# Kernel tuning notes

Hardware: AMD Instinct MI355X
Metric: run time of the kernel (lower is better)

The kernel has to match this reference:

```python
import jax, jax.numpy as jnp
import numpy as np

N = 2048
D0, D1, D2 = 33, 33, 65
O = 128

def setup_inputs() -> dict:
    key = jax.random.key(0)
    k0, k1, k2, kw = jax.random.split(key, 4)
    x0 = jax.random.normal(k0, (N, D0), dtype=jnp.float32)
    x1 = jax.random.normal(k1, (N, D1), dtype=jnp.float32)
    x2 = jax.random.normal(k2, (N, D2), dtype=jnp.float32)
    # xavier_normal for weight_tensor of shape input_sizes + (output_size,):
    # fan_in = D0*D1*D2 treated as receptive field? torch xavier on 4D tensor uses
    # fan_in = shape[1]*receptive, but for faithfulness of *math* any gaussian init works;
    # use std = sqrt(2/(fan_in+fan_out)) with fan computed as torch does for >2D:
    # fan_in = shape[1]*shape[2]*shape[3]? torch: fan_in = size(1)*prod(size()[2:]),
    # fan_out = size(0)*prod(size()[2:]).
    recept = D2 * O
    fan_in = D1 * recept
    fan_out = D0 * recept
    std = float(np.sqrt(2.0 / (fan_in + fan_out)))
    weight_tensor = jax.random.normal(kw, (D0, D1, D2, O), dtype=jnp.float32) * std
    bias = jnp.zeros((O,), dtype=jnp.float32)
    return {"x0": x0, "x1": x1, "x2": x2, "weight_tensor": weight_tensor, "bias": bias}

def reference(x0, x1, x2, weight_tensor, bias):
    # fusion_tensor[n,a,b,c] = x0[n,a]*x1[n,b]*x2[n,c]  (chained outer products)
    # output[n,o] = sum_{a,b,c} fusion[n,a,b,c] * W[a,b,c,o] + bias; dropout(p=0) is identity.
    # Expressed as one fused einsum (same math, avoids HBM round-trip of the big intermediate).
    out = jnp.einsum('na,nb,nc,abco->no', x0, x1, x2, weight_tensor)
    out = jax.nn.relu(out + bias)
    return out
```

## Files before the change

### kernel.cpp

```cpp
#include <hip/hip_runtime.h>
#include <hip/hip_bf16.h>

typedef __attribute__((ext_vector_type(8))) short bf16x8;
typedef __attribute__((ext_vector_type(4))) float f32x4;

#define U_LD 2176
#define K_REAL 2145
#define NKT 34
#define DIM0 33
#define DIM1 33
#define DIM2 65
#define NROW 2048
#define OO 128

__device__ __forceinline__ unsigned short f2bf(float f) {
  union { float f; unsigned u; } v; v.f = f;
  unsigned r = v.u + 0x7fffu + ((v.u >> 16) & 1u);
  return (unsigned short)(r >> 16);
}

#define GLOAD_LDS16(SRC, DST) \
  __builtin_amdgcn_global_load_lds((const __attribute__((address_space(1))) void*)(SRC), \
                                   (__attribute__((address_space(3))) void*)(DST), 16, 0, 0)

__global__ __launch_bounds__(256) void prep_u_kernel(const float* __restrict__ x1,
                                                     const float* __restrict__ x2,
                                                     ushort* __restrict__ U) {
  __shared__ float s1[DIM1], s2[DIM2];
  int n = blockIdx.x;
  int tid = threadIdx.x;
  if (tid < DIM1) s1[tid] = x1[n * DIM1 + tid];
  int t2 = tid - DIM1;
  if (t2 >= 0 && t2 < DIM2) s2[t2] = x2[n * DIM2 + t2];
  __syncthreads();
  for (int k8 = tid; k8 < U_LD / 8; k8 += 256) {
    union { ushort us[8]; uint4 v; } pk;
#pragma unroll
    for (int j = 0; j < 8; ++j) {
      int k = k8 * 8 + j;
      float val = 0.f;
      if (k < K_REAL) { int b = k / DIM2; int c = k - b * DIM2; val = s1[b] * s2[c]; }
      pk.us[j] = f2bf(val);
    }
    *(uint4*)&U[(size_t)n * U_LD + k8 * 8] = pk.v;
  }
}

__global__ __launch_bounds__(256) void prep_wt_kernel(const float* __restrict__ W,
                                                      ushort* __restrict__ Wt) {
  __shared__ ushort s[64][130];
  int a = blockIdx.y;
  int k0 = blockIdx.x * 64;
  int tid = threadIdx.x;
  for (int idx = tid; idx < 64 * 32; idx += 256) {
    int kk = idx >> 5;
    int og = (idx & 31) * 4;
    int k = k0 + kk;
    float4 v = make_float4(0.f, 0.f, 0.f, 0.f);
    if (k < K_REAL) {
      int b = k / DIM2; int c = k - b * DIM2;
      v = *(const float4*)&W[(((size_t)a * DIM1 + b) * DIM2 + c) * OO + og];
    }
    s[kk][og]     = f2bf(v.x);
    s[kk][og + 1] = f2bf(v.y);
    s[kk][og + 2] = f2bf(v.z);
    s[kk][og + 3] = f2bf(v.w);
  }
  __syncthreads();
  int o  = tid >> 1;
  int kh = (tid & 1) * 32;
  union { ushort us[32]; uint4 v[4]; } pk;
#pragma unroll
  for (int j = 0; j < 32; ++j) pk.us[j] = s[kh + j][o];
  uint4* dst = (uint4*)&Wt[((size_t)a * OO + o) * U_LD + k0 + kh];
#pragma unroll
  for (int q = 0; q < 4; ++q) dst[q] = pk.v[q];
}

__global__ __launch_bounds__(256) void gemm_kernel(const ushort* __restrict__ U,
                                                   const ushort* __restrict__ Wt,
                                                   const float* __restrict__ x0,
                                                   float* __restrict__ out) {
  __shared__ ushort lds[12288];

  int tid = threadIdx.x;
  int lane = tid & 63;
  int w = tid >> 6;
  int wr = w >> 1, wc = w & 1;

  int orig = (int)blockIdx.x;
  int logical = (orig & 7) * 132 + (orig >> 3);
  int a = logical >> 5;
  int m = logical & 31;
  int n0 = m * 64;

  int kblk = lane >> 4;
  int r15 = lane & 15;
  int swz = lane & 7;

  f32x4 acc[2][4];
#pragma unroll
  for (int mi = 0; mi < 2; ++mi)
#pragma unroll
    for (int ni = 0; ni < 4; ++ni)
      acc[mi][ni] = (f32x4){0.f, 0.f, 0.f, 0.f};

  const ushort* WtA = Wt + (size_t)a * OO * U_LD;

  for (int t = 0; t < NKT; ++t) {
    int kk = t * 64;
#pragma unroll
    for (int i = 0; i < 2; ++i) {
      int c = i * 256 + tid;
      int row = c >> 3;
      int ss = (c & 7) ^ (row & 7);
      const ushort* src = U + (size_t)(n0 + row) * U_LD + kk + ss * 8;
      GLOAD_LDS16(src, &lds[(size_t)c * 8]);
    }
#pragma unroll
    for (int i = 0; i < 4; ++i) {
      int c = i * 256 + tid;
      int row = c >> 3;
      int ss = (c & 7) ^ (row & 7);
      const ushort* src = WtA + (size_t)row * U_LD + kk + ss * 8;
      GLOAD_LDS16(src, &lds[4096 + (size_t)c * 8]);
    }
    __syncthreads();

#pragma unroll
    for (int ks = 0; ks < 2; ++ks) {
      bf16x8 af[2], bfr[4];
#pragma unroll
      for (int mi = 0; mi < 2; ++mi) {
        int off = (wr * 32 + mi * 16 + r15) * 128 + ((((ks * 4) + kblk) ^ swz) << 4);
        af[mi] = *(const bf16x8*)((const char*)lds + off);
      }
#pragma unroll
      for (int ni = 0; ni < 4; ++ni) {
        int off = 8192 + (wc * 64 + ni * 16 + r15) * 128 + ((((ks * 4) + kblk) ^ swz) << 4);
        bfr[ni] = *(const bf16x8*)((const char*)lds + off);
      }
#pragma unroll
      for (int mi = 0; mi < 2; ++mi)
#pragma unroll
        for (int ni = 0; ni < 4; ++ni)
          acc[mi][ni] = __builtin_amdgcn_mfma_f32_16x16x32_bf16(af[mi], bfr[ni], acc[mi][ni], 0, 0, 0);
    }
    __syncthreads();
  }

  int jrow = (lane >> 4) * 4;
#pragma unroll
  for (int mi = 0; mi < 2; ++mi) {
#pragma unroll
    for (int j = 0; j < 4; ++j) {
      int row = n0 + wr * 32 + mi * 16 + jrow + j;
      float s = x0[(size_t)row * DIM0 + a];
#pragma unroll
      for (int ni = 0; ni < 4; ++ni) {
        int col = wc * 64 + ni * 16 + r15;
        atomicAdd(&out[(size_t)row * OO + col], acc[mi][ni][j] * s);
      }
    }
  }
}

__global__ __launch_bounds__(256) void relu_kernel(float* __restrict__ out,
                                                   const float* __restrict__ bias) {
  int i = blockIdx.x * 256 + threadIdx.x;
  out[i] = fmaxf(out[i] + bias[i & (OO - 1)], 0.f);
}

extern "C" void kernel_launch(void* const* d_in, const int* in_sizes, int n_in,
                              void* d_out, int out_size, void* d_ws, size_t ws_size,
                              hipStream_t stream) {
  const float* x0   = (const float*)d_in[0];
  const float* x1   = (const float*)d_in[1];
  const float* x2   = (const float*)d_in[2];
  const float* W    = (const float*)d_in[3];
  const float* bias = (const float*)d_in[4];
  float* out = (float*)d_out;

  ushort* U  = (ushort*)d_ws;
  ushort* Wt = (ushort*)((char*)d_ws + (size_t)8912896);

  hipMemsetAsync(d_out, 0, (size_t)NROW * OO * sizeof(float), stream);
  prep_u_kernel<<<NROW, 256, 0, stream>>>(x1, x2, U);
  prep_wt_kernel<<<dim3(34, 33), 256, 0, stream>>>(W, Wt);
  gemm_kernel<<<1056, 256, 0, stream>>>(U, Wt, x0, out);
  relu_kernel<<<(NROW * OO) / 256, 256, 0, stream>>>(out, bias);
}
```

Before: 119.9 us.

## Double-buffer LDS tiles in GEMM to overlap global loads with MFMA

Turns the single-buffered GEMM main loop into a two-stage ping-pong pipeline. Async global-to-LDS loads for the next K tile are issued while MFMAs run on the current buffer, with explicit vmcnt waits and raw s_barrier replacing __syncthreads. It also precomputes source pointers and raises wave priority around the MFMA block. The cost is doubled LDS per block, which may reduce occupancy, and the hand-written waitcnt/barrier ordering has to be exactly right for correctness.

Result: faster. 102.5 us (-14.5%).

```diff
diff --git a/kernel.cpp b/kernel.cpp
--- a/kernel.cpp
+++ b/kernel.cpp
@@ -81,7 +81,7 @@
                                                    const ushort* __restrict__ Wt,
                                                    const float* __restrict__ x0,
                                                    float* __restrict__ out) {
-  __shared__ ushort lds[12288];
+  __shared__ ushort lds[2][12288];
 
   int tid = threadIdx.x;
   int lane = tid & 63;
@@ -107,47 +107,74 @@
 
   const ushort* WtA = Wt + (size_t)a * OO * U_LD;
 
-  for (int t = 0; t < NKT; ++t) {
-    int kk = t * 64;
-#pragma unroll
-    for (int i = 0; i < 2; ++i) {
-      int c = i * 256 + tid;
-      int row = c >> 3;
-      int ss = (c & 7) ^ (row & 7);
-      const ushort* src = U + (size_t)(n0 + row) * U_LD + kk + ss * 8;
-      GLOAD_LDS16(src, &lds[(size_t)c * 8]);
-    }
-#pragma unroll
-    for (int i = 0; i < 4; ++i) {
-      int c = i * 256 + tid;
-      int row = c >> 3;
-      int ss = (c & 7) ^ (row & 7);
-      const ushort* src = WtA + (size_t)row * U_LD + kk + ss * 8;
-      GLOAD_LDS16(src, &lds[4096 + (size_t)c * 8]);
-    }
-    __syncthreads();
-
+  int c0 = tid;        int rA0 = c0 >> 3;  int dA0 = c0 * 8;
+  int c1 = 256 + tid;  int rA1 = c1 >> 3;  int dA1 = c1 * 8;
+  const ushort* pA0 = U + (size_t)(n0 + rA0) * U_LD + ((c0 & 7) ^ (rA0 & 7)) * 8;
+  const ushort* pA1 = U + (size_t)(n0 + rA1) * U_LD + ((c1 & 7) ^ (rA1 & 7)) * 8;
+  int cB0 = tid;        int rB0 = cB0 >> 3;  int dB0 = 4096 + cB0 * 8;
+  int cB1 = 256 + tid;  int rB1 = cB1 >> 3;  int dB1 = 4096 + cB1 * 8;
+  int cB2 = 512 + tid;  int rB2 = cB2 >> 3;  int dB2 = 4096 + cB2 * 8;
+  int cB3 = 768 + tid;  int rB3 = cB3 >> 3;  int dB3 = 4096 + cB3 * 8;
+  const ushort* pB0 = WtA + (size_t)rB0 * U_LD + ((cB0 & 7) ^ (rB0 & 7)) * 8;
+  const ushort* pB1 = WtA + (size_t)rB1 * U_LD + ((cB1 & 7) ^ (rB1 & 7)) * 8;
+  const ushort* pB2 = WtA + (size_t)rB2 * U_LD + ((cB2 & 7) ^ (rB2 & 7)) * 8;
+  const ushort* pB3 = WtA + (size_t)rB3 * U_LD + ((cB3 & 7) ^ (rB3 & 7)) * 8;
+
+  auto STAGE = [&](ushort* Lb) {
+    GLOAD_LDS16(pA0, Lb + dA0); pA0 += 64;
+    GLOAD_LDS16(pA1, Lb + dA1); pA1 += 64;
+    GLOAD_LDS16(pB0, Lb + dB0); pB0 += 64;
+    GLOAD_LDS16(pB1, Lb + dB1); pB1 += 64;
+    GLOAD_LDS16(pB2, Lb + dB2); pB2 += 64;
+    GLOAD_LDS16(pB3, Lb + dB3); pB3 += 64;
+  };
+
+  auto COMPUTE = [&](const ushort* Lb) {
+    const char* base = (const char*)Lb;
 #pragma unroll
     for (int ks = 0; ks < 2; ++ks) {
       bf16x8 af[2], bfr[4];
 #pragma unroll
       for (int mi = 0; mi < 2; ++mi) {
         int off = (wr * 32 + mi * 16 + r15) * 128 + ((((ks * 4) + kblk) ^ swz) << 4);
-        af[mi] = *(const bf16x8*)((const char*)lds + off);
+        af[mi] = *(const bf16x8*)(base + off);
       }
 #pragma unroll
       for (int ni = 0; ni < 4; ++ni) {
         int off = 8192 + (wc * 64 + ni * 16 + r15) * 128 + ((((ks * 4) + kblk) ^ swz) << 4);
-        bfr[ni] = *(const bf16x8*)((const char*)lds + off);
+        bfr[ni] = *(const bf16x8*)(base + off);
       }
+      __builtin_amdgcn_s_setprio(1);
 #pragma unroll
       for (int mi = 0; mi < 2; ++mi)
 #pragma unroll
         for (int ni = 0; ni < 4; ++ni)
           acc[mi][ni] = __builtin_amdgcn_mfma_f32_16x16x32_bf16(af[mi], bfr[ni], acc[mi][ni], 0, 0, 0);
-    }
-    __syncthreads();
-  }
+      __builtin_amdgcn_s_setprio(0);
+    }
+  };
+
+  STAGE(&lds[0][0]);
+  STAGE(&lds[1][0]);
+  asm volatile("s_waitcnt vmcnt(6)" ::: "memory");
+  __builtin_amdgcn_s_barrier();
+
+  for (int it = 0; it < 16; ++it) {
+    COMPUTE(&lds[0][0]);
+    __builtin_amdgcn_s_barrier();
+    STAGE(&lds[0][0]);
+    asm volatile("s_waitcnt vmcnt(6)" ::: "memory");
+    __builtin_amdgcn_s_barrier();
+    COMPUTE(&lds[1][0]);
+    __builtin_amdgcn_s_barrier();
+    STAGE(&lds[1][0]);
+    asm volatile("s_waitcnt vmcnt(6)" ::: "memory");
+    __builtin_amdgcn_s_barrier();
+  }
+  COMPUTE(&lds[0][0]);
+  asm volatile("s_waitcnt vmcnt(0)" ::: "memory");
+  __builtin_amdgcn_s_barrier();
+  COMPUTE(&lds[1][0]);
 
   int jrow = (lane >> 4) * 4;
 #pragma unroll
```
